# Performance work log

Measured on AMD Instinct MI355X. Metric: run time of the kernel, lower is better.

The kernel has to match this reference:

```python
import jax, jax.numpy as jnp
import numpy as np

N_NODES = 100000
N_EDGES = 1600000
D = 64  # emb_dim == attn_q_dim == attn_dim


def setup_inputs() -> dict:
    key = jax.random.key(0)
    k1, k2, k3, k4 = jax.random.split(key, 4)
    h = jax.random.normal(k1, (N_NODES, D), dtype=jnp.float32)
    h_attn_q = jax.random.normal(k2, (N_NODES, D), dtype=jnp.float32)
    # attn_lin: Linear(attn_q_dim + attn_dim, 1) -> weight [2D, 1], bias [1]
    W_attn = jax.random.normal(k3, (2 * D, 1), dtype=jnp.float32) * (1.0 / np.sqrt(2 * D))
    b_attn = jnp.zeros((1,), dtype=jnp.float32)
    edge_index = jax.random.randint(k4, (2, N_EDGES), 0, N_NODES, dtype=jnp.int64)
    return {"h": h, "h_attn_q": h_attn_q, "W_attn": W_attn, "b_attn": b_attn,
            "edge_index": edge_index}


def reference(h, h_attn_q, W_attn, b_attn, edge_index):
    """AttnConv (num_relations=1, h_attn=None): per-edge attention score,
    scatter-softmax over destination groups, weighted scatter-add."""
    src = edge_index[0]  # j (message source)
    dst = edge_index[1]  # i (aggregation index)
    n = h.shape[0]
    d_q = h_attn_q.shape[-1]
    # attn_lin(cat([q_i, k_j])) decomposed: score = q_i @ Wq + k_j @ Wk + b
    # (mathematically identical to the concat+linear, avoids [E, 2D] concat)
    alpha_q = h_attn_q @ W_attn[:d_q]          # [N, 1]
    alpha_k = h @ W_attn[d_q:]                 # [N, 1] (h_attn falls back to h_j)
    scores = alpha_q[dst] + alpha_k[src] + b_attn  # [E, 1]
    # scatter softmax over dst groups (PyG softmax(index, ptr, size_i))
    seg_max = jax.ops.segment_max(scores, dst, num_segments=n)  # [N, 1]
    e = jnp.exp(scores - seg_max[dst])
    seg_sum = jax.ops.segment_sum(e, dst, num_segments=n)       # [N, 1]
    a = e / (seg_sum[dst] + 1e-16)                               # [E, 1]
    # weighted scatter-add of messages h_j * a_j
    out = jax.ops.segment_sum(h[src] * a, dst, num_segments=n)   # [N, D]
    return out
```

## Files before the change

### kernel.cpp

```cpp
#include <hip/hip_runtime.h>
#include <hip/hip_fp16.h>
#include <cstdint>
#include <math.h>

#define EMB_D 64
#define BUCKET_BITS 7
#define BUCKET_NODES 128
#define MAXB 1024
#define STRIDE 2560
#define SORT_CAP STRIDE
#define NT 512
#define REG_E 7

__global__ __launch_bounds__(NT, 8)
void k_pp(const float* __restrict__ h, const float* __restrict__ W,
          const int* __restrict__ src, const int* __restrict__ dst,
          float* __restrict__ Ak, __half* __restrict__ h16,
          int* __restrict__ brel, unsigned* __restrict__ packed,
          int n_nodes, int n_edges, int part_blocks) {
    __shared__ int lh[MAXB], cur[MAXB];
    int tid = threadIdx.x;
    if (blockIdx.x < (unsigned)part_blocks) {
        int per = (n_edges + part_blocks - 1) / part_blocks;
        int e0 = blockIdx.x * per;
        int e1 = min(e0 + per, n_edges);
        lh[tid] = 0; lh[tid + NT] = 0;
        __syncthreads();
        uint2 ed[REG_E];
#pragma unroll
        for (int i = 0; i < REG_E; ++i) {
            int e = e0 + i * NT + tid;
            if (e < e1) {
                int d = dst[e];
                ed[i] = make_uint2((unsigned)src[e], (unsigned)d);
                atomicAdd(&lh[d >> BUCKET_BITS], 1);
            } else {
                ed[i] = make_uint2(0u, 0xFFFFFFFFu);
            }
        }
        __syncthreads();
        for (int b = tid; b < MAXB; b += NT) {
            int c = lh[b];
            cur[b] = c ? (b * STRIDE + atomicAdd(&brel[b], c)) : 0;
        }
        __syncthreads();
#pragma unroll
        for (int i = 0; i < REG_E; ++i) {
            if (ed[i].y != 0xFFFFFFFFu) {
                int d  = (int)ed[i].y;
                int bk = d >> BUCKET_BITS;
                int pos = atomicAdd(&cur[bk], 1);
                if (pos < (bk + 1) * STRIDE)
                    packed[pos] = (ed[i].x << BUCKET_BITS)
                                | (unsigned)(d & (BUCKET_NODES - 1));
            }
        }
    } else {
        long long gid = (long long)(blockIdx.x - part_blocks) * NT + tid;
        int node = (int)(gid >> 4);
        int q    = (int)(gid & 15);
        if (node < n_nodes) {
            const float4* hp = (const float4*)(h + ((long long)node << 6));
            float4 hv = hp[q];
            __half2 p01, p23;
            p01.x = __float2half(hv.x); p01.y = __float2half(hv.y);
            p23.x = __float2half(hv.z); p23.y = __float2half(hv.w);
            uint2 pw;
            pw.x = *(const unsigned*)&p01; pw.y = *(const unsigned*)&p23;
            ((uint2*)(h16 + ((long long)node << 6)))[q] = pw;
            float4 wv = ((const float4*)(W + EMB_D))[q];
            float vk = hv.x * wv.x + hv.y * wv.y + hv.z * wv.z + hv.w * wv.w;
#pragma unroll
            for (int o = 8; o > 0; o >>= 1) vk += __shfl_xor(vk, o, 64);
            if (q == 0) Ak[node] = __expf(vk);
        }
    }
}

__global__ __launch_bounds__(NT, 8)
void k_fused5(const unsigned* __restrict__ packed, const int* __restrict__ brel,
              const float* __restrict__ Ak, const __half* __restrict__ h16,
              float* __restrict__ out, int n_nodes) {
    __shared__ unsigned stageRaw[SORT_CAP];
    __shared__ uint2 spair[SORT_CAP];
    __shared__ int cnt[BUCKET_NODES], cur[BUCKET_NODES], rstart[BUCKET_NODES];
    __shared__ short order_[BUCKET_NODES];
    int bk    = blockIdx.x;
    int node0 = bk << BUCKET_BITS;
    int nloc  = min(BUCKET_NODES, n_nodes - node0);
    int beg   = bk * STRIDE;
    int cntE  = min(brel[bk], SORT_CAP);
    int tid = threadIdx.x;

    if (tid < BUCKET_NODES) cnt[tid] = 0;
    if (tid == 0 && cntE == 0) spair[0] = make_uint2(0u, 0u);
    __syncthreads();
    for (int i = tid; i < cntE; i += NT) {
        unsigned p = packed[beg + i];
        stageRaw[i] = p;
        atomicAdd(&cnt[p & (BUCKET_NODES - 1)], 1);
    }
    __syncthreads();
    if (tid < BUCKET_NODES) cur[tid] = cnt[tid];
    __syncthreads();
    for (int off = 1; off < BUCKET_NODES; off <<= 1) {
        int t = 0;
        if (tid < BUCKET_NODES && tid >= off) t = cur[tid - off];
        __syncthreads();
        if (tid < BUCKET_NODES) cur[tid] += t;
        __syncthreads();
    }
    if (tid < BUCKET_NODES) {
        int excl = cur[tid] - cnt[tid];
        rstart[tid] = excl;
        cur[tid]    = excl;
    }
    __syncthreads();
    for (int i = tid; i < cntE; i += NT) {
        unsigned p = stageRaw[i];
        unsigned s = p >> BUCKET_BITS;
        int pos = atomicAdd(&cur[p & (BUCKET_NODES - 1)], 1);
        spair[pos] = make_uint2(s, __float_as_uint(Ak[s]));
    }
    if (tid < 64) {
        int L = tid;
        int r0 = (cnt[L]      << 8) | L;
        int r1 = (cnt[L + 64] << 8) | (L + 64);
        for (int k = 2; k <= 128; k <<= 1) {
            for (int j = k >> 1; j >= 1; j >>= 1) {
                if (j < 64) {
                    int q0 = __shfl_xor(r0, j, 64);
                    int q1 = __shfl_xor(r1, j, 64);
                    bool lower = ((L & j) == 0);
                    bool up0 = ((L & k) == 0);
                    bool up1 = (((L + 64) & k) == 0);
                    r0 = (up0 == lower) ? min(r0, q0) : max(r0, q0);
                    r1 = (up1 == lower) ? min(r1, q1) : max(r1, q1);
                } else {
                    int lo = min(r0, r1), hi = max(r0, r1);
                    r0 = lo; r1 = hi;
                }
            }
        }
        order_[L]      = (short)(r0 & (BUCKET_NODES - 1));
        order_[L + 64] = (short)(r1 & (BUCKET_NODES - 1));
    }
    __syncthreads();

    int wave = tid >> 6, lane = tid & 63;
    int oct = lane >> 3, ol = lane & 7;
    int cntE_m1 = (cntE > 0) ? (cntE - 1) : 0;
#pragma unroll
    for (int pass = 0; pass < 2; ++pass) {
        int g = pass ? (15 - wave) : wave;
        int dl    = (int)order_[g * 8 + oct];
        int start = rstart[dl], cN = cnt[dl];
        int cmax  = cnt[(int)order_[g * 8 + 7]];
        float a0=0.f,a1=0.f,a2=0.f,a3=0.f,a4=0.f,a5=0.f,a6=0.f,a7=0.f,l=0.f;
        int j = 0;
        for (; j + 3 < cmax; j += 4) {
            int i0 = min(start + ((j     < cN) ? j     : 0), cntE_m1);
            int i1 = min(start + ((j + 1 < cN) ? j + 1 : 0), cntE_m1);
            int i2 = min(start + ((j + 2 < cN) ? j + 2 : 0), cntE_m1);
            int i3 = min(start + ((j + 3 < cN) ? j + 3 : 0), cntE_m1);
            uint2 sp0 = spair[i0];
            uint2 sp1 = spair[i1];
            uint2 sp2 = spair[i2];
            uint2 sp3 = spair[i3];
            uint4 v0 = ((const uint4*)(h16 + ((long long)sp0.x << 6)))[ol];
            uint4 v1 = ((const uint4*)(h16 + ((long long)sp1.x << 6)))[ol];
            uint4 v2 = ((const uint4*)(h16 + ((long long)sp2.x << 6)))[ol];
            uint4 v3 = ((const uint4*)(h16 + ((long long)sp3.x << 6)))[ol];
            float p0 = (j     < cN) ? __uint_as_float(sp0.y) : 0.f;
            float p1 = (j + 1 < cN) ? __uint_as_float(sp1.y) : 0.f;
            float p2 = (j + 2 < cN) ? __uint_as_float(sp2.y) : 0.f;
            float p3 = (j + 3 < cN) ? __uint_as_float(sp3.y) : 0.f;
            float2 f0, f1, f2, f3;
            f0 = __half22float2(*(const __half2*)&v0.x);
            f1 = __half22float2(*(const __half2*)&v0.y);
            f2 = __half22float2(*(const __half2*)&v0.z);
            f3 = __half22float2(*(const __half2*)&v0.w);
            a0 = fmaf(p0, f0.x, a0); a1 = fmaf(p0, f0.y, a1);
            a2 = fmaf(p0, f1.x, a2); a3 = fmaf(p0, f1.y, a3);
            a4 = fmaf(p0, f2.x, a4); a5 = fmaf(p0, f2.y, a5);
            a6 = fmaf(p0, f3.x, a6); a7 = fmaf(p0, f3.y, a7);
            l += p0;
            f0 = __half22float2(*(const __half2*)&v1.x);
            f1 = __half22float2(*(const __half2*)&v1.y);
            f2 = __half22float2(*(const __half2*)&v1.z);
            f3 = __half22float2(*(const __half2*)&v1.w);
            a0 = fmaf(p1, f0.x, a0); a1 = fmaf(p1, f0.y, a1);
            a2 = fmaf(p1, f1.x, a2); a3 = fmaf(p1, f1.y, a3);
            a4 = fmaf(p1, f2.x, a4); a5 = fmaf(p1, f2.y, a5);
            a6 = fmaf(p1, f3.x, a6); a7 = fmaf(p1, f3.y, a7);
            l += p1;
            f0 = __half22float2(*(const __half2*)&v2.x);
            f1 = __half22float2(*(const __half2*)&v2.y);
            f2 = __half22float2(*(const __half2*)&v2.z);
            f3 = __half22float2(*(const __half2*)&v2.w);
            a0 = fmaf(p2, f0.x, a0); a1 = fmaf(p2, f0.y, a1);
            a2 = fmaf(p2, f1.x, a2); a3 = fmaf(p2, f1.y, a3);
            a4 = fmaf(p2, f2.x, a4); a5 = fmaf(p2, f2.y, a5);
            a6 = fmaf(p2, f3.x, a6); a7 = fmaf(p2, f3.y, a7);
            l += p2;
            f0 = __half22float2(*(const __half2*)&v3.x);
            f1 = __half22float2(*(const __half2*)&v3.y);
            f2 = __half22float2(*(const __half2*)&v3.z);
            f3 = __half22float2(*(const __half2*)&v3.w);
            a0 = fmaf(p3, f0.x, a0); a1 = fmaf(p3, f0.y, a1);
            a2 = fmaf(p3, f1.x, a2); a3 = fmaf(p3, f1.y, a3);
            a4 = fmaf(p3, f2.x, a4); a5 = fmaf(p3, f2.y, a5);
            a6 = fmaf(p3, f3.x, a6); a7 = fmaf(p3, f3.y, a7);
            l += p3;
        }
        for (; j < cmax; ++j) {
            int i0 = min(start + ((j < cN) ? j : 0), cntE_m1);
            uint2 sp0 = spair[i0];
            float p0 = (j < cN) ? __uint_as_float(sp0.y) : 0.f;
            uint4 v0 = ((const uint4*)(h16 + ((long long)sp0.x << 6)))[ol];
            float2 f0 = __half22float2(*(const __half2*)&v0.x);
            float2 f1 = __half22float2(*(const __half2*)&v0.y);
            float2 f2 = __half22float2(*(const __half2*)&v0.z);
            float2 f3 = __half22float2(*(const __half2*)&v0.w);
            a0 = fmaf(p0, f0.x, a0); a1 = fmaf(p0, f0.y, a1);
            a2 = fmaf(p0, f1.x, a2); a3 = fmaf(p0, f1.y, a3);
            a4 = fmaf(p0, f2.x, a4); a5 = fmaf(p0, f2.y, a5);
            a6 = fmaf(p0, f3.x, a6); a7 = fmaf(p0, f3.y, a7);
            l += p0;
        }
        if (dl < nloc) {
            float inv = 1.f / (l + 1e-16f);
            float4* orow = (float4*)(out + ((long long)(node0 + dl) << 6));
            orow[ol * 2]     = make_float4(a0 * inv, a1 * inv, a2 * inv, a3 * inv);
            orow[ol * 2 + 1] = make_float4(a4 * inv, a5 * inv, a6 * inv, a7 * inv);
        }
    }
}

extern "C" void kernel_launch(void* const* d_in, const int* in_sizes, int n_in,
                              void* d_out, int out_size, void* d_ws, size_t ws_size,
                              hipStream_t stream) {
    const float* h  = (const float*)d_in[0];
    const float* W  = (const float*)d_in[2];
    const int*   ei = (const int*)d_in[4];

    int n_nodes = in_sizes[0] / EMB_D;
    int n_edges = in_sizes[4] / 2;
    const int* src = ei;
    const int* dst = ei + n_edges;
    float* out = (float*)d_out;

    int n_buckets = (n_nodes + BUCKET_NODES - 1) >> BUCKET_BITS;

    float*    Ak     = (float*)d_ws;
    int*      brel   = (int*)(Ak + n_nodes);
    unsigned* packed = (unsigned*)(brel + MAXB);
    char*     p_end  = (char*)(packed + (size_t)n_buckets * STRIDE);
    __half*   h16    = (__half*)((char*)d_ws +
                       (((size_t)(p_end - (char*)d_ws) + 15) & ~(size_t)15));

    hipMemsetAsync(brel, 0, MAXB * sizeof(int), stream);

    int part_blocks = (n_edges + REG_E * NT - 1) / (REG_E * NT);
    if (part_blocks < 512) part_blocks = 512;
    int prep_blocks = (int)(((long long)n_nodes * 16 + NT - 1) / NT);
    k_pp<<<part_blocks + prep_blocks, NT, 0, stream>>>(h, W, src, dst, Ak, h16,
                                                       brel, packed,
                                                       n_nodes, n_edges, part_blocks);

    k_fused5<<<n_buckets, NT, 0, stream>>>(packed, brel, Ak, h16, out, n_nodes);
}
```

Baseline: 158.6 us.

## Split each 128-node bucket across two 256-thread blocks handling 64 nodes each

```diff
diff --git a/kernel.cpp b/kernel.cpp
--- a/kernel.cpp
+++ b/kernel.cpp
@@ -8,8 +8,10 @@
 #define BUCKET_NODES 128
 #define MAXB 1024
 #define STRIDE 2560
-#define SORT_CAP STRIDE
+#define HALF_NODES 64
+#define SPAIR_CAP 1280
 #define NT 512
+#define FNT 256
 #define REG_E 7
 
 __global__ __launch_bounds__(NT, 8)
@@ -77,92 +79,89 @@
     }
 }
 
-__global__ __launch_bounds__(NT, 8)
-void k_fused5(const unsigned* __restrict__ packed, const int* __restrict__ brel,
+__global__ __launch_bounds__(FNT, 7)
+void k_fused6(const unsigned* __restrict__ packed, const int* __restrict__ brel,
               const float* __restrict__ Ak, const __half* __restrict__ h16,
               float* __restrict__ out, int n_nodes) {
-    __shared__ unsigned stageRaw[SORT_CAP];
-    __shared__ uint2 spair[SORT_CAP];
-    __shared__ int cnt[BUCKET_NODES], cur[BUCKET_NODES], rstart[BUCKET_NODES];
-    __shared__ short order_[BUCKET_NODES];
-    int bk    = blockIdx.x;
-    int node0 = bk << BUCKET_BITS;
-    int nloc  = min(BUCKET_NODES, n_nodes - node0);
-    int beg   = bk * STRIDE;
-    int cntE  = min(brel[bk], SORT_CAP);
+    __shared__ unsigned stageRaw[STRIDE];
+    __shared__ uint2 spair[SPAIR_CAP];
+    __shared__ int cnt[HALF_NODES], cur[HALF_NODES], rstart[HALF_NODES];
+    __shared__ short order_[HALF_NODES];
+    int coarse = blockIdx.x >> 1;
+    int half   = blockIdx.x & 1;
+    int node0  = (coarse << BUCKET_BITS) + half * HALF_NODES;
+    int nloc   = min(HALF_NODES, n_nodes - node0);
+    int beg    = coarse * STRIDE;
+    int cntE   = min(brel[coarse], STRIDE);
     int tid = threadIdx.x;
 
-    if (tid < BUCKET_NODES) cnt[tid] = 0;
-    if (tid == 0 && cntE == 0) spair[0] = make_uint2(0u, 0u);
-    __syncthreads();
-    for (int i = tid; i < cntE; i += NT) {
+    if (tid < HALF_NODES) cnt[tid] = 0;
+    if (tid == 0) spair[0] = make_uint2(0u, 0u);
+    __syncthreads();
+    for (int i = tid; i < cntE; i += FNT) {
         unsigned p = packed[beg + i];
         stageRaw[i] = p;
-        atomicAdd(&cnt[p & (BUCKET_NODES - 1)], 1);
-    }
-    __syncthreads();
-    if (tid < BUCKET_NODES) cur[tid] = cnt[tid];
-    __syncthreads();
-    for (int off = 1; off < BUCKET_NODES; off <<= 1) {
+        unsigned loc = p & (BUCKET_NODES - 1);
+        if ((int)(loc >> 6) == half) atomicAdd(&cnt[loc & (HALF_NODES - 1)], 1);
+    }
+    __syncthreads();
+    if (tid < HALF_NODES) cur[tid] = cnt[tid];
+    __syncthreads();
+    for (int off = 1; off < HALF_NODES; off <<= 1) {
         int t = 0;
-        if (tid < BUCKET_NODES && tid >= off) t = cur[tid - off];
-        __syncthreads();
-        if (tid < BUCKET_NODES) cur[tid] += t;
-        __syncthreads();
-    }
-    if (tid < BUCKET_NODES) {
+        if (tid < HALF_NODES && tid >= off) t = cur[tid - off];
+        __syncthreads();
+        if (tid < HALF_NODES) cur[tid] += t;
+        __syncthreads();
+    }
+    if (tid < HALF_NODES) {
         int excl = cur[tid] - cnt[tid];
         rstart[tid] = excl;
         cur[tid]    = excl;
     }
     __syncthreads();
-    for (int i = tid; i < cntE; i += NT) {
+    for (int i = tid; i < cntE; i += FNT) {
         unsigned p = stageRaw[i];
-        unsigned s = p >> BUCKET_BITS;
-        int pos = atomicAdd(&cur[p & (BUCKET_NODES - 1)], 1);
-        spair[pos] = make_uint2(s, __float_as_uint(Ak[s]));
+        unsigned loc = p & (BUCKET_NODES - 1);
+        if ((int)(loc >> 6) == half) {
+            unsigned s = p >> BUCKET_BITS;
+            int pos = atomicAdd(&cur[loc & (HALF_NODES - 1)], 1);
+            if (pos < SPAIR_CAP)
+                spair[pos] = make_uint2(s, __float_as_uint(Ak[s]));
+        }
     }
     if (tid < 64) {
         int L = tid;
-        int r0 = (cnt[L]      << 8) | L;
-        int r1 = (cnt[L + 64] << 8) | (L + 64);
-        for (int k = 2; k <= 128; k <<= 1) {
+        int r0 = (cnt[L] << 6) | L;
+        for (int k = 2; k <= 64; k <<= 1) {
             for (int j = k >> 1; j >= 1; j >>= 1) {
-                if (j < 64) {
-                    int q0 = __shfl_xor(r0, j, 64);
-                    int q1 = __shfl_xor(r1, j, 64);
-                    bool lower = ((L & j) == 0);
-                    bool up0 = ((L & k) == 0);
-                    bool up1 = (((L + 64) & k) == 0);
-                    r0 = (up0 == lower) ? min(r0, q0) : max(r0, q0);
-                    r1 = (up1 == lower) ? min(r1, q1) : max(r1, q1);
-                } else {
-                    int lo = min(r0, r1), hi = max(r0, r1);
-                    r0 = lo; r1 = hi;
-                }
+                int q0 = __shfl_xor(r0, j, 64);
+                bool lower = ((L & j) == 0);
+                bool up0 = ((L & k) == 0);
+                r0 = (up0 == lower) ? min(r0, q0) : max(r0, q0);
             }
         }
-        order_[L]      = (short)(r0 & (BUCKET_NODES - 1));
-        order_[L + 64] = (short)(r1 & (BUCKET_NODES - 1));
+        order_[L] = (short)(r0 & (HALF_NODES - 1));
     }
     __syncthreads();
 
     int wave = tid >> 6, lane = tid & 63;
     int oct = lane >> 3, ol = lane & 7;
-    int cntE_m1 = (cntE > 0) ? (cntE - 1) : 0;
+    int hcnt = rstart[HALF_NODES - 1] + cnt[HALF_NODES - 1];
+    int hc_m1 = (hcnt > 0) ? min(hcnt, SPAIR_CAP) - 1 : 0;
 #pragma unroll
     for (int pass = 0; pass < 2; ++pass) {
-        int g = pass ? (15 - wave) : wave;
+        int g = pass ? (7 - wave) : wave;
         int dl    = (int)order_[g * 8 + oct];
         int start = rstart[dl], cN = cnt[dl];
         int cmax  = cnt[(int)order_[g * 8 + 7]];
         float a0=0.f,a1=0.f,a2=0.f,a3=0.f,a4=0.f,a5=0.f,a6=0.f,a7=0.f,l=0.f;
         int j = 0;
         for (; j + 3 < cmax; j += 4) {
-            int i0 = min(start + ((j     < cN) ? j     : 0), cntE_m1);
-            int i1 = min(start + ((j + 1 < cN) ? j + 1 : 0), cntE_m1);
-            int i2 = min(start + ((j + 2 < cN) ? j + 2 : 0), cntE_m1);
-            int i3 = min(start + ((j + 3 < cN) ? j + 3 : 0), cntE_m1);
+            int i0 = min(start + ((j     < cN) ? j     : 0), hc_m1);
+            int i1 = min(start + ((j + 1 < cN) ? j + 1 : 0), hc_m1);
+            int i2 = min(start + ((j + 2 < cN) ? j + 2 : 0), hc_m1);
+            int i3 = min(start + ((j + 3 < cN) ? j + 3 : 0), hc_m1);
             uint2 sp0 = spair[i0];
             uint2 sp1 = spair[i1];
             uint2 sp2 = spair[i2];
@@ -214,7 +213,7 @@
             l += p3;
         }
         for (; j < cmax; ++j) {
-            int i0 = min(start + ((j < cN) ? j : 0), cntE_m1);
+            int i0 = min(start + ((j < cN) ? j : 0), hc_m1);
             uint2 sp0 = spair[i0];
             float p0 = (j < cN) ? __uint_as_float(sp0.y) : 0.f;
             uint4 v0 = ((const uint4*)(h16 + ((long long)sp0.x << 6)))[ol];
@@ -268,5 +267,5 @@
                                                        brel, packed,
                                                        n_nodes, n_edges, part_blocks);
 
-    k_fused5<<<n_buckets, NT, 0, stream>>>(packed, brel, Ak, h16, out, n_nodes);
+    k_fused6<<<n_buckets * 2, FNT, 0, stream>>>(packed, brel, Ak, h16, out, n_nodes);
 }
```

Measured after the change: 159.6 us. Within noise of the previous version (+0.6%).

## Partition edges into 512-node superbuckets with block-local staging for coalesced writes

Applied to the files above, without the earlier changes.

```diff
diff --git a/kernel.cpp b/kernel.cpp
--- a/kernel.cpp
+++ b/kernel.cpp
@@ -4,11 +4,12 @@
 #include <math.h>
 
 #define EMB_D 64
-#define BUCKET_BITS 7
 #define BUCKET_NODES 128
-#define MAXB 1024
-#define STRIDE 2560
-#define SORT_CAP STRIDE
+#define SBITS 9
+#define SNODES 512
+#define MAXS 256
+#define SSTRIDE 9984
+#define SPAIR_CAP 2560
 #define NT 512
 #define REG_E 7
 
@@ -16,15 +17,16 @@
 void k_pp(const float* __restrict__ h, const float* __restrict__ W,
           const int* __restrict__ src, const int* __restrict__ dst,
           float* __restrict__ Ak, __half* __restrict__ h16,
-          int* __restrict__ brel, unsigned* __restrict__ packed,
+          int* __restrict__ brelp, unsigned* __restrict__ packed,
           int n_nodes, int n_edges, int part_blocks) {
-    __shared__ int lh[MAXB], cur[MAXB];
+    __shared__ int lh[MAXS], lb[MAXS], lcur[MAXS], gb[MAXS];
+    __shared__ unsigned stg[REG_E * NT];
     int tid = threadIdx.x;
     if (blockIdx.x < (unsigned)part_blocks) {
         int per = (n_edges + part_blocks - 1) / part_blocks;
         int e0 = blockIdx.x * per;
         int e1 = min(e0 + per, n_edges);
-        lh[tid] = 0; lh[tid + NT] = 0;
+        if (tid < MAXS) lh[tid] = 0;
         __syncthreads();
         uint2 ed[REG_E];
 #pragma unroll
@@ -33,26 +35,45 @@
             if (e < e1) {
                 int d = dst[e];
                 ed[i] = make_uint2((unsigned)src[e], (unsigned)d);
-                atomicAdd(&lh[d >> BUCKET_BITS], 1);
+                atomicAdd(&lh[d >> SBITS], 1);
             } else {
                 ed[i] = make_uint2(0u, 0xFFFFFFFFu);
             }
         }
         __syncthreads();
-        for (int b = tid; b < MAXB; b += NT) {
-            int c = lh[b];
-            cur[b] = c ? (b * STRIDE + atomicAdd(&brel[b], c)) : 0;
+        int cnt_s = (tid < MAXS) ? lh[tid] : 0;
+        for (int off = 1; off < MAXS; off <<= 1) {
+            int t = 0;
+            if (tid < MAXS && tid >= off) t = lh[tid - off];
+            __syncthreads();
+            if (tid < MAXS) lh[tid] += t;
+            __syncthreads();
+        }
+        if (tid < MAXS) {
+            int lbase = lh[tid] - cnt_s;
+            lb[tid]   = lbase;
+            lcur[tid] = lbase;
+            gb[tid]   = cnt_s ? (tid * SSTRIDE + atomicAdd(&brelp[tid << 4], cnt_s)) : 0;
         }
         __syncthreads();
 #pragma unroll
         for (int i = 0; i < REG_E; ++i) {
             if (ed[i].y != 0xFFFFFFFFu) {
-                int d  = (int)ed[i].y;
-                int bk = d >> BUCKET_BITS;
-                int pos = atomicAdd(&cur[bk], 1);
-                if (pos < (bk + 1) * STRIDE)
-                    packed[pos] = (ed[i].x << BUCKET_BITS)
-                                | (unsigned)(d & (BUCKET_NODES - 1));
+                int d = (int)ed[i].y;
+                int s = d >> SBITS;
+                int pos = atomicAdd(&lcur[s], 1);
+                stg[pos] = (ed[i].x << SBITS) | (unsigned)(d & (SNODES - 1));
+            }
+        }
+        __syncthreads();
+        int gid = tid >> 3, l8 = tid & 7;
+        for (int s = gid; s < MAXS; s += 64) {
+            int b0 = lb[s], b1 = lcur[s];
+            int g0 = gb[s];
+            int lim = (s + 1) * SSTRIDE;
+            for (int p = b0 + l8; p < b1; p += 8) {
+                int gp = g0 + (p - b0);
+                if (gp < lim) packed[gp] = stg[p];
             }
         }
     } else {
@@ -78,27 +99,28 @@
 }
 
 __global__ __launch_bounds__(NT, 8)
-void k_fused5(const unsigned* __restrict__ packed, const int* __restrict__ brel,
+void k_fused7(const unsigned* __restrict__ packed, const int* __restrict__ brelp,
               const float* __restrict__ Ak, const __half* __restrict__ h16,
               float* __restrict__ out, int n_nodes) {
-    __shared__ unsigned stageRaw[SORT_CAP];
-    __shared__ uint2 spair[SORT_CAP];
+    __shared__ uint2 spair[SPAIR_CAP];
     __shared__ int cnt[BUCKET_NODES], cur[BUCKET_NODES], rstart[BUCKET_NODES];
     __shared__ short order_[BUCKET_NODES];
-    int bk    = blockIdx.x;
-    int node0 = bk << BUCKET_BITS;
-    int nloc  = min(BUCKET_NODES, n_nodes - node0);
-    int beg   = bk * STRIDE;
-    int cntE  = min(brel[bk], SORT_CAP);
+    int bk      = blockIdx.x;
+    int super   = bk >> 2;
+    int quarter = bk & 3;
+    int node0   = bk << 7;
+    int nloc    = min(BUCKET_NODES, n_nodes - node0);
+    int sbeg    = super * SSTRIDE;
+    int cntS    = min(brelp[super << 4], SSTRIDE);
     int tid = threadIdx.x;
 
     if (tid < BUCKET_NODES) cnt[tid] = 0;
-    if (tid == 0 && cntE == 0) spair[0] = make_uint2(0u, 0u);
-    __syncthreads();
-    for (int i = tid; i < cntE; i += NT) {
-        unsigned p = packed[beg + i];
-        stageRaw[i] = p;
-        atomicAdd(&cnt[p & (BUCKET_NODES - 1)], 1);
+    if (tid == 0) spair[0] = make_uint2(0u, 0u);
+    __syncthreads();
+    for (int i = tid; i < cntS; i += NT) {
+        unsigned p = packed[sbeg + i];
+        unsigned loc = p & (SNODES - 1);
+        if ((int)(loc >> 7) == quarter) atomicAdd(&cnt[loc & (BUCKET_NODES - 1)], 1);
     }
     __syncthreads();
     if (tid < BUCKET_NODES) cur[tid] = cnt[tid];
@@ -116,11 +138,15 @@
         cur[tid]    = excl;
     }
     __syncthreads();
-    for (int i = tid; i < cntE; i += NT) {
-        unsigned p = stageRaw[i];
-        unsigned s = p >> BUCKET_BITS;
-        int pos = atomicAdd(&cur[p & (BUCKET_NODES - 1)], 1);
-        spair[pos] = make_uint2(s, __float_as_uint(Ak[s]));
+    for (int i = tid; i < cntS; i += NT) {
+        unsigned p = packed[sbeg + i];
+        unsigned loc = p & (SNODES - 1);
+        if ((int)(loc >> 7) == quarter) {
+            unsigned s = p >> SBITS;
+            int pos = atomicAdd(&cur[loc & (BUCKET_NODES - 1)], 1);
+            if (pos < SPAIR_CAP)
+                spair[pos] = make_uint2(s, __float_as_uint(Ak[s]));
+        }
     }
     if (tid < 64) {
         int L = tid;
@@ -149,7 +175,8 @@
 
     int wave = tid >> 6, lane = tid & 63;
     int oct = lane >> 3, ol = lane & 7;
-    int cntE_m1 = (cntE > 0) ? (cntE - 1) : 0;
+    int hcnt = rstart[BUCKET_NODES - 1] + cnt[BUCKET_NODES - 1];
+    int hc_m1 = (hcnt > 0) ? min(hcnt, SPAIR_CAP) - 1 : 0;
 #pragma unroll
     for (int pass = 0; pass < 2; ++pass) {
         int g = pass ? (15 - wave) : wave;
@@ -159,10 +186,10 @@
         float a0=0.f,a1=0.f,a2=0.f,a3=0.f,a4=0.f,a5=0.f,a6=0.f,a7=0.f,l=0.f;
         int j = 0;
         for (; j + 3 < cmax; j += 4) {
-            int i0 = min(start + ((j     < cN) ? j     : 0), cntE_m1);
-            int i1 = min(start + ((j + 1 < cN) ? j + 1 : 0), cntE_m1);
-            int i2 = min(start + ((j + 2 < cN) ? j + 2 : 0), cntE_m1);
-            int i3 = min(start + ((j + 3 < cN) ? j + 3 : 0), cntE_m1);
+            int i0 = min(start + ((j     < cN) ? j     : 0), hc_m1);
+            int i1 = min(start + ((j + 1 < cN) ? j + 1 : 0), hc_m1);
+            int i2 = min(start + ((j + 2 < cN) ? j + 2 : 0), hc_m1);
+            int i3 = min(start + ((j + 3 < cN) ? j + 3 : 0), hc_m1);
             uint2 sp0 = spair[i0];
             uint2 sp1 = spair[i1];
             uint2 sp2 = spair[i2];
@@ -214,7 +241,7 @@
             l += p3;
         }
         for (; j < cmax; ++j) {
-            int i0 = min(start + ((j < cN) ? j : 0), cntE_m1);
+            int i0 = min(start + ((j < cN) ? j : 0), hc_m1);
             uint2 sp0 = spair[i0];
             float p0 = (j < cN) ? __uint_as_float(sp0.y) : 0.f;
             uint4 v0 = ((const uint4*)(h16 + ((long long)sp0.x << 6)))[ol];
@@ -250,23 +277,23 @@
     const int* dst = ei + n_edges;
     float* out = (float*)d_out;
 
-    int n_buckets = (n_nodes + BUCKET_NODES - 1) >> BUCKET_BITS;
+    int n_buckets = (n_nodes + BUCKET_NODES - 1) >> 7;
 
     float*    Ak     = (float*)d_ws;
-    int*      brel   = (int*)(Ak + n_nodes);
-    unsigned* packed = (unsigned*)(brel + MAXB);
-    char*     p_end  = (char*)(packed + (size_t)n_buckets * STRIDE);
+    int*      brelp  = (int*)(Ak + n_nodes);
+    unsigned* packed = (unsigned*)(brelp + MAXS * 16);
+    char*     p_end  = (char*)(packed + (size_t)MAXS * SSTRIDE);
     __half*   h16    = (__half*)((char*)d_ws +
                        (((size_t)(p_end - (char*)d_ws) + 15) & ~(size_t)15));
 
-    hipMemsetAsync(brel, 0, MAXB * sizeof(int), stream);
+    hipMemsetAsync(brelp, 0, MAXS * 16 * sizeof(int), stream);
 
     int part_blocks = (n_edges + REG_E * NT - 1) / (REG_E * NT);
     if (part_blocks < 512) part_blocks = 512;
     int prep_blocks = (int)(((long long)n_nodes * 16 + NT - 1) / NT);
     k_pp<<<part_blocks + prep_blocks, NT, 0, stream>>>(h, W, src, dst, Ak, h16,
-                                                       brel, packed,
+                                                       brelp, packed,
                                                        n_nodes, n_edges, part_blocks);
 
-    k_fused5<<<n_buckets, NT, 0, stream>>>(packed, brel, Ak, h16, out, n_nodes);
+    k_fused7<<<n_buckets, NT, 0, stream>>>(packed, brelp, Ak, h16, out, n_nodes);
 }
```

Measured after the change: 161.5 us. About the same (+1.8%).

## Stage partitioned edges in shared memory and pad bucket counters

Applied to the files above, without the earlier changes.

```diff
diff --git a/kernel.cpp b/kernel.cpp
--- a/kernel.cpp
+++ b/kernel.cpp
@@ -10,15 +10,17 @@
 #define STRIDE 2560
 #define SORT_CAP STRIDE
 #define NT 512
-#define REG_E 7
-
-__global__ __launch_bounds__(NT, 8)
+#define PARTB 256
+#define REG_E 13
+
+__global__ __launch_bounds__(NT, 4)
 void k_pp(const float* __restrict__ h, const float* __restrict__ W,
           const int* __restrict__ src, const int* __restrict__ dst,
           float* __restrict__ Ak, __half* __restrict__ h16,
-          int* __restrict__ brel, unsigned* __restrict__ packed,
+          int* __restrict__ brelp, unsigned* __restrict__ packed,
           int n_nodes, int n_edges, int part_blocks) {
-    __shared__ int lh[MAXB], cur[MAXB];
+    __shared__ int lh[MAXB], lb[MAXB], lcur[MAXB], gb[MAXB];
+    __shared__ unsigned stg[REG_E * NT];
     int tid = threadIdx.x;
     if (blockIdx.x < (unsigned)part_blocks) {
         int per = (n_edges + part_blocks - 1) / part_blocks;
@@ -39,9 +41,22 @@
             }
         }
         __syncthreads();
-        for (int b = tid; b < MAXB; b += NT) {
-            int c = lh[b];
-            cur[b] = c ? (b * STRIDE + atomicAdd(&brel[b], c)) : 0;
+        int o1 = lh[tid], o2 = lh[tid + NT];
+        for (int off = 1; off < MAXB; off <<= 1) {
+            int a1 = (tid >= off) ? lh[tid - off] : 0;
+            int a2 = lh[tid + NT - off];
+            __syncthreads();
+            lh[tid] += a1; lh[tid + NT] += a2;
+            __syncthreads();
+        }
+        {
+            int b1 = lh[tid] - o1,  b2 = lh[tid + NT] - o2;
+            lb[tid] = b1;            lb[tid + NT] = b2;
+            lcur[tid] = b1;          lcur[tid + NT] = b2;
+            gb[tid]      = o1 ? (tid * STRIDE
+                                 + atomicAdd(&brelp[tid << 4], o1)) : 0;
+            gb[tid + NT] = o2 ? ((tid + NT) * STRIDE
+                                 + atomicAdd(&brelp[(tid + NT) << 4], o2)) : 0;
         }
         __syncthreads();
 #pragma unroll
@@ -49,10 +64,20 @@
             if (ed[i].y != 0xFFFFFFFFu) {
                 int d  = (int)ed[i].y;
                 int bk = d >> BUCKET_BITS;
-                int pos = atomicAdd(&cur[bk], 1);
-                if (pos < (bk + 1) * STRIDE)
-                    packed[pos] = (ed[i].x << BUCKET_BITS)
-                                | (unsigned)(d & (BUCKET_NODES - 1));
+                int pos = atomicAdd(&lcur[bk], 1);
+                stg[pos] = (ed[i].x << BUCKET_BITS)
+                         | (unsigned)(d & (BUCKET_NODES - 1));
+            }
+        }
+        __syncthreads();
+        int grp = tid >> 2, l4 = tid & 3;
+        for (int b = grp; b < MAXB; b += 128) {
+            int s0 = lb[b], s1 = lcur[b];
+            int g0 = gb[b];
+            int lim = (b + 1) * STRIDE;
+            for (int p = s0 + l4; p < s1; p += 4) {
+                int gp = g0 + (p - s0);
+                if (gp < lim) packed[gp] = stg[p];
             }
         }
     } else {
@@ -78,7 +103,7 @@
 }
 
 __global__ __launch_bounds__(NT, 8)
-void k_fused5(const unsigned* __restrict__ packed, const int* __restrict__ brel,
+void k_fused5(const unsigned* __restrict__ packed, const int* __restrict__ brelp,
               const float* __restrict__ Ak, const __half* __restrict__ h16,
               float* __restrict__ out, int n_nodes) {
     __shared__ unsigned stageRaw[SORT_CAP];
@@ -89,7 +114,7 @@
     int node0 = bk << BUCKET_BITS;
     int nloc  = min(BUCKET_NODES, n_nodes - node0);
     int beg   = bk * STRIDE;
-    int cntE  = min(brel[bk], SORT_CAP);
+    int cntE  = min(brelp[bk << 4], SORT_CAP);
     int tid = threadIdx.x;
 
     if (tid < BUCKET_NODES) cnt[tid] = 0;
@@ -253,20 +278,18 @@
     int n_buckets = (n_nodes + BUCKET_NODES - 1) >> BUCKET_BITS;
 
     float*    Ak     = (float*)d_ws;
-    int*      brel   = (int*)(Ak + n_nodes);
-    unsigned* packed = (unsigned*)(brel + MAXB);
+    int*      brelp  = (int*)(Ak + n_nodes);
+    unsigned* packed = (unsigned*)(brelp + MAXB * 16);
     char*     p_end  = (char*)(packed + (size_t)n_buckets * STRIDE);
     __half*   h16    = (__half*)((char*)d_ws +
                        (((size_t)(p_end - (char*)d_ws) + 15) & ~(size_t)15));
 
-    hipMemsetAsync(brel, 0, MAXB * sizeof(int), stream);
-
-    int part_blocks = (n_edges + REG_E * NT - 1) / (REG_E * NT);
-    if (part_blocks < 512) part_blocks = 512;
+    hipMemsetAsync(brelp, 0, MAXB * 16 * sizeof(int), stream);
+
     int prep_blocks = (int)(((long long)n_nodes * 16 + NT - 1) / NT);
-    k_pp<<<part_blocks + prep_blocks, NT, 0, stream>>>(h, W, src, dst, Ak, h16,
-                                                       brel, packed,
-                                                       n_nodes, n_edges, part_blocks);
-
-    k_fused5<<<n_buckets, NT, 0, stream>>>(packed, brel, Ak, h16, out, n_nodes);
+    k_pp<<<PARTB + prep_blocks, NT, 0, stream>>>(h, W, src, dst, Ak, h16,
+                                                 brelp, packed,
+                                                 n_nodes, n_edges, PARTB);
+
+    k_fused5<<<n_buckets, NT, 0, stream>>>(packed, brelp, Ak, h16, out, n_nodes);
 }
```

Result: no change. 156.6 us (-1.2%).
